# Kernel optimization log

Hardware: AMD Instinct MI355X
Metric: run time of the kernel (lower is better)

The kernel has to match this reference:

```python
import jax, jax.numpy as jnp
import numpy as np

N_NODES = 100000
N_EDGES = 500000
NODE_IN = 16
HID = 128
EDGE_IN = 1
NUM_STACKED = 4  # layers 1..4 share shapes; layer 0 maps NODE_IN -> HID


def setup_inputs() -> dict:
    key = jax.random.key(0)
    ks = jax.random.split(key, 16)

    def p(k, shape, fan_in):
        return (jax.random.normal(k, shape, dtype=jnp.float32) / np.float32(np.sqrt(fan_in)))

    inp = {}
    inp["x"] = jax.random.normal(ks[0], (N_NODES, NODE_IN), dtype=jnp.float32)
    inp["edge_index"] = jax.random.randint(ks[1], (2, N_EDGES), 0, N_NODES)
    inp["edge_attr"] = jax.random.normal(ks[2], (N_EDGES, EDGE_IN), dtype=jnp.float32)
    # GINE layer 0 (NODE_IN -> HID): edge lin maps EDGE_IN -> NODE_IN (PyG GINEConv.lin)
    inp["We0"] = p(ks[3], (EDGE_IN, NODE_IN), EDGE_IN)
    inp["be0"] = jnp.zeros((NODE_IN,), jnp.float32)
    inp["W10"] = p(ks[4], (NODE_IN, HID), NODE_IN)
    inp["b10"] = jnp.zeros((HID,), jnp.float32)
    inp["W20"] = p(ks[5], (HID, HID), HID)
    inp["b20"] = jnp.zeros((HID,), jnp.float32)
    # GINE layers 1..4 (HID -> HID), stacked on leading axis
    inp["We_s"] = p(ks[6], (NUM_STACKED, EDGE_IN, HID), EDGE_IN)
    inp["be_s"] = jnp.zeros((NUM_STACKED, HID), jnp.float32)
    inp["W1_s"] = p(ks[7], (NUM_STACKED, HID, HID), HID)
    inp["b1_s"] = jnp.zeros((NUM_STACKED, HID), jnp.float32)
    inp["W2_s"] = p(ks[8], (NUM_STACKED, HID, HID), HID)
    inp["b2_s"] = jnp.zeros((NUM_STACKED, HID), jnp.float32)
    # edge predictor: Linear(2*HID, HID) -> ELU -> Linear(HID, 1)
    inp["Wp1"] = p(ks[9], (2 * HID, HID), 2 * HID)
    inp["bp1"] = jnp.zeros((HID,), jnp.float32)
    inp["Wp2"] = p(ks[10], (HID, 1), HID)
    inp["bp2"] = jnp.zeros((1,), jnp.float32)
    return inp


def _gine(x, src, dst, eattr, We, be, W1, b1, W2, b2):
    # PyG GINEConv: aggr_i = sum_{(j->i)} ReLU(x_j + lin(edge_attr)); out = nn((1+eps)*x + aggr), eps=0
    m = jax.nn.relu(x[src] + eattr @ We + be)                 # [E, d] gathered messages
    aggr = jax.ops.segment_sum(m, dst, num_segments=x.shape[0])  # scatter-add to targets
    h = x + aggr
    return jax.nn.elu(h @ W1 + b1) @ W2 + b2                  # nn = Linear-ELU-Linear


def reference(x, edge_index, edge_attr, We0, be0, W10, b10, W20, b20,
              We_s, be_s, W1_s, b1_s, W2_s, b2_s, Wp1, bp1, Wp2, bp2):
    src, dst = edge_index[0], edge_index[1]
    # dropout is identity at inference (eval mode)
    h = jax.nn.elu(_gine(x, src, dst, edge_attr, We0, be0, W10, b10, W20, b20))
    for l in range(NUM_STACKED):
        h = jax.nn.elu(_gine(h, src, dst, edge_attr,
                             We_s[l], be_s[l], W1_s[l], b1_s[l], W2_s[l], b2_s[l]))
    ef = jnp.concatenate([h[src], h[dst]], axis=1)            # [E, 2*HID]
    out = jax.nn.elu(ef @ Wp1 + bp1) @ Wp2 + bp2              # [E, 1]
    return out[:, 0]
```

## Files before the change

kernel.cpp:

```cpp
#include <hip/hip_runtime.h>

#define N_NODES 100000
#define N_EDGES 500000
#define NODE_IN 16
#define HID 128
#define LPAD 140
#define SCAN_CHUNK 1024
#define NB_SCAN ((N_NODES + SCAN_CHUNK - 1) / SCAN_CHUNK)
#define DBINS 1024
#define NBLK64 1563
#define PERM_PAD (NBLK64 * 64)

typedef __attribute__((ext_vector_type(8))) short short8;
typedef __attribute__((ext_vector_type(4))) float f32x4;

__device__ __forceinline__ float elu_f(float v) {
    return v > 0.f ? v : __expf(v) - 1.f;
}

__device__ __forceinline__ unsigned short f2b(float f) {
    unsigned int u = __float_as_uint(f);
    unsigned int r = (u + 0x7fffu + ((u >> 16) & 1u)) >> 16;
    return (unsigned short)r;
}
__device__ __forceinline__ float b2f(unsigned short h) {
    return __uint_as_float((unsigned int)h << 16);
}
__device__ __forceinline__ unsigned short f2h(float f) {
    _Float16 h = (_Float16)f;
    unsigned short u;
    __builtin_memcpy(&u, &h, 2);
    return u;
}
__device__ __forceinline__ float h2f(unsigned short u) {
    _Float16 h;
    __builtin_memcpy(&h, &u, 2);
    return (float)h;
}

__global__ void deg_count_kernel(const int* __restrict__ ei, int* __restrict__ deg) {
    int e = blockIdx.x * 256 + threadIdx.x;
    if (e < N_EDGES) atomicAdd(&deg[ei[N_EDGES + e]], 1);
}

__global__ __launch_bounds__(1024) void scanA_kernel(const int* __restrict__ deg, int* __restrict__ bsum) {
    __shared__ int s[SCAN_CHUNK];
    int i = blockIdx.x * SCAN_CHUNK + threadIdx.x;
    s[threadIdx.x] = (i < N_NODES) ? deg[i] : 0;
    __syncthreads();
    for (int off = SCAN_CHUNK / 2; off > 0; off >>= 1) {
        if (threadIdx.x < off) s[threadIdx.x] += s[threadIdx.x + off];
        __syncthreads();
    }
    if (threadIdx.x == 0) bsum[blockIdx.x] = s[0];
}

__global__ void scanB_kernel(const int* __restrict__ bsum, int* __restrict__ boff,
                             int* __restrict__ rowPtr) {
    if (threadIdx.x == 0 && blockIdx.x == 0) {
        int r = 0;
        for (int i = 0; i < NB_SCAN; i++) { boff[i] = r; r += bsum[i]; }
        rowPtr[N_NODES] = N_EDGES;
    }
}

__global__ __launch_bounds__(1024) void scanC_kernel(const int* __restrict__ deg,
                                                     const int* __restrict__ boff,
                                                     int* __restrict__ rowPtr,
                                                     int* __restrict__ cursor) {
    __shared__ int bufA[SCAN_CHUNK], bufB[SCAN_CHUNK];
    int i = blockIdx.x * SCAN_CHUNK + threadIdx.x;
    int t = threadIdx.x;
    bufA[t] = (i < N_NODES) ? deg[i] : 0;
    __syncthreads();
    int* src = bufA; int* dst = bufB;
    for (int off = 1; off < SCAN_CHUNK; off <<= 1) {
        dst[t] = (t >= off) ? (src[t - off] + src[t]) : src[t];
        __syncthreads();
        int* tmp = src; src = dst; dst = tmp;
    }
    if (i < N_NODES) {
        int excl = (t == 0) ? 0 : src[t - 1];
        int v = excl + boff[blockIdx.x];
        rowPtr[i] = v;
        cursor[i] = v;
    }
}

__global__ void fill_kernel(const int* __restrict__ ei, const float* __restrict__ ea,
                            int* __restrict__ cursor, int2* __restrict__ edgeP) {
    int e = blockIdx.x * 256 + threadIdx.x;
    if (e < N_EDGES) {
        int d = ei[N_EDGES + e];
        int p = atomicAdd(&cursor[d], 1);
        edgeP[p] = make_int2(ei[e], __float_as_int(ea[e]));
    }
}

__global__ __launch_bounds__(1024) void s1_blockhist_kernel(const int* __restrict__ deg,
                                                            int* __restrict__ blockHist) {
    __shared__ int h[DBINS];
    int t = threadIdx.x, b = blockIdx.x;
    h[t] = 0;
    __syncthreads();
    int i = b * SCAN_CHUNK + t;
    if (i < N_NODES) atomicAdd(&h[min(deg[i], DBINS - 1)], 1);
    __syncthreads();
    blockHist[b * DBINS + t] = h[t];
}

__global__ __launch_bounds__(256) void s2a_colscan_kernel(int* __restrict__ blockHist,
                                                          int* __restrict__ binTot) {
    int k = blockIdx.x * 256 + threadIdx.x;
    if (k >= DBINS) return;
    int r = 0;
#pragma unroll 7
    for (int b = 0; b < NB_SCAN; b++) {
        int v = blockHist[b * DBINS + k];
        blockHist[b * DBINS + k] = r;
        r += v;
    }
    binTot[k] = r;
}

__global__ __launch_bounds__(1024) void s2b_binscan_kernel(const int* __restrict__ binTot,
                                                           int* __restrict__ binStart) {
    __shared__ int bufA[DBINS], bufB[DBINS];
    int k = threadIdx.x;
    bufA[k] = binTot[k];
    __syncthreads();
    int* src = bufA; int* dst = bufB;
    for (int off = 1; off < DBINS; off <<= 1) {
        dst[k] = (k >= off) ? (src[k - off] + src[k]) : src[k];
        __syncthreads();
        int* tmp = src; src = dst; dst = tmp;
    }
    binStart[k] = (k == 0) ? 0 : src[k - 1];
}

__global__ __launch_bounds__(1024) void s2c_add_kernel(int* __restrict__ blockHist,
                                                       const int* __restrict__ binStart) {
    int g = blockIdx.x * 1024 + threadIdx.x;
    if (g < NB_SCAN * DBINS) blockHist[g] += binStart[g & (DBINS - 1)];
}

__global__ __launch_bounds__(1024) void s3_scatter_kernel(const int* __restrict__ deg,
                                                          const int* __restrict__ blockHist,
                                                          int* __restrict__ perm) {
    __shared__ int cur[DBINS];
    int t = threadIdx.x, b = blockIdx.x;
    cur[t] = blockHist[b * DBINS + t];
    __syncthreads();
    int i = b * SCAN_CHUNK + t;
    if (i < N_NODES) {
        int k = min(deg[i], DBINS - 1);
        int p = atomicAdd(&cur[k], 1);
        perm[p] = i;
    }
}

__global__ __launch_bounds__(256) void pack_w_kernel(const float* __restrict__ W, int K_off,
                                                     unsigned short* __restrict__ hi,
                                                     unsigned short* __restrict__ lo)
{
    int gid = blockIdx.x * 256 + threadIdx.x;
    if (gid >= 4 * 8 * 64) return;
    int lane = gid & 63, tl = (gid >> 6) & 7, ch = gid >> 9;
    int kb = ch * 32 + (lane >> 4) * 8;
    int n  = tl * 16 + (lane & 15);
    for (int j = 0; j < 8; j++) {
        float w = W[(size_t)(K_off + kb + j) * 128 + n];
        unsigned short h = f2b(w);
        hi[(size_t)gid * 8 + j] = h;
        lo[(size_t)gid * 8 + j] = f2b(w - b2f(h));
    }
}

__global__ __launch_bounds__(256) void scatter0_kernel(
    const float* __restrict__ x, const int* __restrict__ ei,
    const float* __restrict__ ea, const float* __restrict__ We0,
    const float* __restrict__ be0, float* __restrict__ aggr)
{
    int idx = blockIdx.x * 256 + threadIdx.x;
    int e = idx >> 4, c = idx & 15;
    int s = ei[e], d = ei[N_EDGES + e];
    float m = x[s * NODE_IN + c] + ea[e] * We0[c] + be0[c];
    m = fmaxf(m, 0.f);
    atomicAdd(&aggr[d * NODE_IN + c], m);
}

__device__ __forceinline__ void fma4x4(float (&acc)[4][4],
    const float4& r0, const float4& r1, const float4& r2, const float4& r3,
    const float4& w0, const float4& w1, const float4& w2, const float4& w3)
{
    float r[4][4] = {{r0.x, r0.y, r0.z, r0.w}, {r1.x, r1.y, r1.z, r1.w},
                     {r2.x, r2.y, r2.z, r2.w}, {r3.x, r3.y, r3.z, r3.w}};
    float w[4][4] = {{w0.x, w0.y, w0.z, w0.w}, {w1.x, w1.y, w1.z, w1.w},
                     {w2.x, w2.y, w2.z, w2.w}, {w3.x, w3.y, w3.z, w3.w}};
#pragma unroll
    for (int i = 0; i < 4; i++)
#pragma unroll
        for (int k = 0; k < 4; k++)
#pragma unroll
            for (int c = 0; c < 4; c++)
                acc[i][c] = fmaf(r[i][k], w[k][c], acc[i][c]);
}

__global__ __launch_bounds__(256) void mlp0_kernel(
    const float* __restrict__ x, const float* __restrict__ aggr,
    const float* __restrict__ W1, const float* __restrict__ b1,
    const float* __restrict__ W2, const float* __restrict__ b2,
    unsigned short* __restrict__ h)
{
    __shared__ float in0[32][20];
    __shared__ float mid[32][HID];
    const int t = threadIdx.x;
    const int q = t & 31, g = t >> 5;
    const int c0 = q * 4;
    const int base = blockIdx.x * 32;

    for (int i = t; i < 32 * NODE_IN; i += 256) {
        int r = i >> 4, cc = i & 15;
        int n = base + r;
        in0[r][cc] = x[n * NODE_IN + cc] + aggr[n * NODE_IN + cc];
    }
    __syncthreads();

    float4 bb = *(const float4*)&b1[c0];
    float acc[4][4];
#pragma unroll
    for (int i = 0; i < 4; i++) { acc[i][0] = bb.x; acc[i][1] = bb.y; acc[i][2] = bb.z; acc[i][3] = bb.w; }
    for (int k = 0; k < NODE_IN; k += 4) {
        float4 r0 = *(const float4*)&in0[g * 4 + 0][k];
        float4 r1 = *(const float4*)&in0[g * 4 + 1][k];
        float4 r2 = *(const float4*)&in0[g * 4 + 2][k];
        float4 r3 = *(const float4*)&in0[g * 4 + 3][k];
        float4 w0 = *(const float4*)&W1[(k + 0) * HID + c0];
        float4 w1 = *(const float4*)&W1[(k + 1) * HID + c0];
        float4 w2 = *(const float4*)&W1[(k + 2) * HID + c0];
        float4 w3 = *(const float4*)&W1[(k + 3) * HID + c0];
        fma4x4(acc, r0, r1, r2, r3, w0, w1, w2, w3);
    }
#pragma unroll
    for (int i = 0; i < 4; i++)
        *(float4*)&mid[g * 4 + i][c0] = make_float4(elu_f(acc[i][0]), elu_f(acc[i][1]),
                                                    elu_f(acc[i][2]), elu_f(acc[i][3]));
    __syncthreads();

    float4 bb2 = *(const float4*)&b2[c0];
    float acc2[4][4];
#pragma unroll
    for (int i = 0; i < 4; i++) { acc2[i][0] = bb2.x; acc2[i][1] = bb2.y; acc2[i][2] = bb2.z; acc2[i][3] = bb2.w; }
    for (int k = 0; k < HID; k += 4) {
        float4 r0 = *(const float4*)&mid[g * 4 + 0][k];
        float4 r1 = *(const float4*)&mid[g * 4 + 1][k];
        float4 r2 = *(const float4*)&mid[g * 4 + 2][k];
        float4 r3 = *(const float4*)&mid[g * 4 + 3][k];
        float4 w0 = *(const float4*)&W2[(k + 0) * HID + c0];
        float4 w1 = *(const float4*)&W2[(k + 1) * HID + c0];
        float4 w2 = *(const float4*)&W2[(k + 2) * HID + c0];
        float4 w3 = *(const float4*)&W2[(k + 3) * HID + c0];
        fma4x4(acc2, r0, r1, r2, r3, w0, w1, w2, w3);
    }
#pragma unroll
    for (int i = 0; i < 4; i++) {
        ushort4 o;
        o.x = f2h(elu_f(acc2[i][0])); o.y = f2h(elu_f(acc2[i][1]));
        o.z = f2h(elu_f(acc2[i][2])); o.w = f2h(elu_f(acc2[i][3]));
        *(ushort4*)&h[(size_t)(base + g * 4 + i) * HID + c0] = o;
    }
}

__device__ __forceinline__ void afrag_split(const float (&buf)[16][LPAD], int lane,
                                            short8 (&ah)[4], short8 (&al)[4])
{
    const int m = lane & 15, s8 = (lane >> 4) * 8;
#pragma unroll
    for (int ch = 0; ch < 4; ch++) {
        float4 a0 = *(const float4*)&buf[m][ch * 32 + s8];
        float4 a1 = *(const float4*)&buf[m][ch * 32 + s8 + 4];
        float av[8] = {a0.x, a0.y, a0.z, a0.w, a1.x, a1.y, a1.z, a1.w};
#pragma unroll
        for (int j = 0; j < 8; j++) {
            unsigned short h = f2b(av[j]);
            ah[ch][j] = (short)h;
            al[ch][j] = (short)f2b(av[j] - b2f(h));
        }
    }
}

template <bool PRED>
__global__ __launch_bounds__(256, 4) void gine_mfma_kernel(
    const unsigned short* __restrict__ hin, const int* __restrict__ rowPtr,
    const int2* __restrict__ edgeP, const int* __restrict__ perm,
    const float* __restrict__ We, const float* __restrict__ be,
    const unsigned short* __restrict__ W1h, const unsigned short* __restrict__ W1l,
    const float* __restrict__ b1,
    const unsigned short* __restrict__ W2h, const unsigned short* __restrict__ W2l,
    const float* __restrict__ b2,
    unsigned short* __restrict__ hout,
    const unsigned short* __restrict__ P1h, const unsigned short* __restrict__ P1l,
    const unsigned short* __restrict__ P2h, const unsigned short* __restrict__ P2l,
    unsigned short* __restrict__ Pbuf)
{
    __shared__ float bufAll[4][16][LPAD];
    const int w = threadIdx.x >> 6;
    const int lane = threadIdx.x & 63;
    float (&buf)[16][LPAD] = bufAll[w];
    const int qg = lane & 15, rg = lane >> 4;
    const int c0 = qg * 8;
    const int base = blockIdx.x * 64 + w * 16;

    float wev[8], bev[8];
#pragma unroll
    for (int j = 0; j < 8; j++) { wev[j] = We[c0 + j]; bev[j] = be[c0 + j]; }

    int nn[4], s0[4], e0[4];
    float acc[4][8];
#pragma unroll
    for (int i = 0; i < 4; i++) {
        nn[i] = perm[base + rg * 4 + i];
        s0[i] = rowPtr[nn[i]];
        e0[i] = rowPtr[nn[i] + 1];
        short8 h0 = *(const short8*)&hin[(size_t)nn[i] * HID + c0];
#pragma unroll
        for (int j = 0; j < 8; j++) acc[i][j] = h2f((unsigned short)h0[j]);
    }
    int maxd = 0;
#pragma unroll
    for (int i = 0; i < 4; i++) maxd = max(maxd, e0[i] - s0[i]);

    int idx[8]; float av[8]; bool act[8];
#pragma unroll
    for (int u = 0; u < 2; u++)
#pragma unroll
        for (int i = 0; i < 4; i++) {
            int slot = u * 4 + i;
            int j = s0[i] + u;
            act[slot] = j < e0[i];
            int jc = act[slot] ? j : (N_EDGES - 1);
            int2 ep = edgeP[jc];
            idx[slot] = ep.x;
            av[slot]  = __int_as_float(ep.y);
        }

    for (int sb = 0; sb < maxd; sb += 2) {
        short8 hraw[8];
#pragma unroll
        for (int s = 0; s < 8; s++)
            hraw[s] = *(const short8*)&hin[(size_t)idx[s] * HID + c0];

        int nidx[8]; float nav[8]; bool nact[8];
#pragma unroll
        for (int u = 0; u < 2; u++)
#pragma unroll
            for (int i = 0; i < 4; i++) {
                int slot = u * 4 + i;
                int j = s0[i] + sb + 2 + u;
                nact[slot] = j < e0[i];
                int jc = nact[slot] ? j : (N_EDGES - 1);
                int2 ep = edgeP[jc];
                nidx[slot] = ep.x;
                nav[slot]  = __int_as_float(ep.y);
            }

#pragma unroll
        for (int u = 0; u < 2; u++)
#pragma unroll
            for (int i = 0; i < 4; i++) {
                int slot = u * 4 + i;
                if (act[slot]) {
#pragma unroll
                    for (int j = 0; j < 8; j++) {
                        float hv = h2f((unsigned short)hraw[slot][j]);
                        acc[i][j] += fmaxf(fmaf(av[slot], wev[j], bev[j]) + hv, 0.f);
                    }
                }
            }
#pragma unroll
        for (int s = 0; s < 8; s++) {
            idx[s] = nidx[s]; av[s] = nav[s]; act[s] = nact[s];
        }
    }
#pragma unroll
    for (int i = 0; i < 4; i++) {
        *(float4*)&buf[rg * 4 + i][c0]     = make_float4(acc[i][0], acc[i][1], acc[i][2], acc[i][3]);
        *(float4*)&buf[rg * 4 + i][c0 + 4] = make_float4(acc[i][4], acc[i][5], acc[i][6], acc[i][7]);
    }
    __syncthreads();

    const int col16 = lane & 15, r0 = (lane >> 4) * 4;

    {
        short8 ah[4], al[4];
        afrag_split(buf, lane, ah, al);
        float res[8][4];
#pragma unroll
        for (int tl = 0; tl < 8; tl++) {
            int col = tl * 16 + col16;
            float bv = b1[col];
            f32x4 c = {bv, bv, bv, bv};
#pragma unroll
            for (int ch = 0; ch < 4; ch++) {
                int off = ((ch * 8 + tl) * 64 + lane) * 8;
                short8 bh = *(const short8*)&W1h[off];
                short8 bl = *(const short8*)&W1l[off];
                c = __builtin_amdgcn_mfma_f32_16x16x32_bf16(ah[ch], bh, c, 0, 0, 0);
                c = __builtin_amdgcn_mfma_f32_16x16x32_bf16(al[ch], bh, c, 0, 0, 0);
                c = __builtin_amdgcn_mfma_f32_16x16x32_bf16(ah[ch], bl, c, 0, 0, 0);
            }
#pragma unroll
            for (int r = 0; r < 4; r++) res[tl][r] = elu_f(c[r]);
        }
        __syncthreads();
#pragma unroll
        for (int tl = 0; tl < 8; tl++)
#pragma unroll
            for (int r = 0; r < 4; r++)
                buf[r0 + r][tl * 16 + col16] = res[tl][r];
    }
    __syncthreads();

    {
        short8 ah[4], al[4];
        afrag_split(buf, lane, ah, al);
        float res[8][4];
#pragma unroll
        for (int tl = 0; tl < 8; tl++) {
            int col = tl * 16 + col16;
            float bv = b2[col];
            f32x4 c = {bv, bv, bv, bv};
#pragma unroll
            for (int ch = 0; ch < 4; ch++) {
                int off = ((ch * 8 + tl) * 64 + lane) * 8;
                short8 bh = *(const short8*)&W2h[off];
                short8 bl = *(const short8*)&W2l[off];
                c = __builtin_amdgcn_mfma_f32_16x16x32_bf16(ah[ch], bh, c, 0, 0, 0);
                c = __builtin_amdgcn_mfma_f32_16x16x32_bf16(al[ch], bh, c, 0, 0, 0);
                c = __builtin_amdgcn_mfma_f32_16x16x32_bf16(ah[ch], bl, c, 0, 0, 0);
            }
#pragma unroll
            for (int r = 0; r < 4; r++) res[tl][r] = elu_f(c[r]);
        }
        __syncthreads();
#pragma unroll
        for (int tl = 0; tl < 8; tl++)
#pragma unroll
            for (int r = 0; r < 4; r++)
                buf[r0 + r][tl * 16 + col16] = res[tl][r];
    }
    __syncthreads();

    if constexpr (!PRED) {
#pragma unroll
        for (int i = 0; i < 4; i++) {
            short8 o;
#pragma unroll
            for (int j = 0; j < 8; j++) o[j] = (short)f2h(buf[rg * 4 + i][c0 + j]);
            *(short8*)&hout[(size_t)nn[i] * HID + c0] = o;
        }
    } else {
        short8 ah[4], al[4];
        afrag_split(buf, lane, ah, al);
        int pn[4];
#pragma unroll
        for (int r = 0; r < 4; r++) pn[r] = perm[base + r0 + r];
#pragma unroll
        for (int tl = 0; tl < 8; tl++) {
            int col = tl * 16 + col16;
            f32x4 c1 = {0.f, 0.f, 0.f, 0.f};
            f32x4 c2 = {0.f, 0.f, 0.f, 0.f};
#pragma unroll
            for (int ch = 0; ch < 4; ch++) {
                int off = ((ch * 8 + tl) * 64 + lane) * 8;
                short8 bh1 = *(const short8*)&P1h[off];
                short8 bl1 = *(const short8*)&P1l[off];
                c1 = __builtin_amdgcn_mfma_f32_16x16x32_bf16(ah[ch], bh1, c1, 0, 0, 0);
                c1 = __builtin_amdgcn_mfma_f32_16x16x32_bf16(al[ch], bh1, c1, 0, 0, 0);
                c1 = __builtin_amdgcn_mfma_f32_16x16x32_bf16(ah[ch], bl1, c1, 0, 0, 0);
                short8 bh2 = *(const short8*)&P2h[off];
                short8 bl2 = *(const short8*)&P2l[off];
                c2 = __builtin_amdgcn_mfma_f32_16x16x32_bf16(ah[ch], bh2, c2, 0, 0, 0);
                c2 = __builtin_amdgcn_mfma_f32_16x16x32_bf16(al[ch], bh2, c2, 0, 0, 0);
                c2 = __builtin_amdgcn_mfma_f32_16x16x32_bf16(ah[ch], bl2, c2, 0, 0, 0);
            }
#pragma unroll
            for (int r = 0; r < 4; r++) {
                size_t n = (size_t)pn[r];
                Pbuf[n * 256 + col]       = f2b(c1[r]);
                Pbuf[n * 256 + 128 + col] = f2b(c2[r]);
            }
        }
    }
}

__global__ __launch_bounds__(256) void pred_edge_kernel(
    const unsigned short* __restrict__ Pbuf, const int* __restrict__ ei,
    const float* __restrict__ bp1, const float* __restrict__ Wp2,
    const float* __restrict__ bp2, float* __restrict__ out)
{
    const int t = threadIdx.x;
    const int lane = t & 31;
    const int eloc = t >> 5;
    const int e = blockIdx.x * 8 + eloc;
    const int c0 = lane * 4;

    int s = ei[e], d = ei[N_EDGES + e];
    ushort4 ua = *(const ushort4*)&Pbuf[(size_t)s * 256 + c0];
    ushort4 ub = *(const ushort4*)&Pbuf[(size_t)d * 256 + 128 + c0];
    float4 bb = *(const float4*)&bp1[c0];
    float4 w = *(const float4*)&Wp2[c0];
    float r = elu_f(b2f(ua.x) + b2f(ub.x) + bb.x) * w.x
            + elu_f(b2f(ua.y) + b2f(ub.y) + bb.y) * w.y
            + elu_f(b2f(ua.z) + b2f(ub.z) + bb.z) * w.z
            + elu_f(b2f(ua.w) + b2f(ub.w) + bb.w) * w.w;
#pragma unroll
    for (int off = 16; off > 0; off >>= 1) r += __shfl_down(r, off, 32);
    if (lane == 0) out[e] = r + bp2[0];
}

extern "C" void kernel_launch(void* const* d_in, const int* in_sizes, int n_in,
                              void* d_out, int out_size, void* d_ws, size_t ws_size,
                              hipStream_t stream) {
    const float* x    = (const float*)d_in[0];
    const int*   ei   = (const int*)d_in[1];
    const float* ea   = (const float*)d_in[2];
    const float* We0  = (const float*)d_in[3];
    const float* be0  = (const float*)d_in[4];
    const float* W10  = (const float*)d_in[5];
    const float* b10  = (const float*)d_in[6];
    const float* W20  = (const float*)d_in[7];
    const float* b20  = (const float*)d_in[8];
    const float* We_s = (const float*)d_in[9];
    const float* be_s = (const float*)d_in[10];
    const float* W1_s = (const float*)d_in[11];
    const float* b1_s = (const float*)d_in[12];
    const float* W2_s = (const float*)d_in[13];
    const float* b2_s = (const float*)d_in[14];
    const float* Wp1  = (const float*)d_in[15];
    const float* bp1  = (const float*)d_in[16];
    const float* Wp2  = (const float*)d_in[17];
    const float* bp2  = (const float*)d_in[18];
    float* out = (float*)d_out;

    unsigned short* h16A = (unsigned short*)d_ws;
    unsigned short* h16B = h16A + (size_t)N_NODES * HID;
    unsigned short* Pbuf = h16B + (size_t)N_NODES * HID;
    float* R = (float*)(Pbuf + (size_t)N_NODES * 256);

    float* aggr0 = R;
    int* deg     = (int*)(aggr0 + (size_t)N_NODES * NODE_IN);
    int* rowPtr  = deg + N_NODES;
    int* cursor  = rowPtr + N_NODES + 1;
    int2* edgeP  = (int2*)(cursor + N_NODES);
    int* bsum    = (int*)(edgeP + N_EDGES);
    int* boff    = bsum + NB_SCAN;
    int* perm    = boff + NB_SCAN;
    int* blockHist = perm + PERM_PAD;
    int* binTot   = blockHist + NB_SCAN * DBINS;
    int* binStart = binTot + DBINS;

    unsigned short* wpk = (unsigned short*)(R + (size_t)6 * 1024 * 1024);
    const size_t WSLOT = 16384;

    hipMemsetAsync(deg, 0, N_NODES * sizeof(int), stream);
    deg_count_kernel<<<(N_EDGES + 255) / 256, 256, 0, stream>>>(ei, deg);
    scanA_kernel<<<NB_SCAN, SCAN_CHUNK, 0, stream>>>(deg, bsum);
    scanB_kernel<<<1, 64, 0, stream>>>(bsum, boff, rowPtr);
    scanC_kernel<<<NB_SCAN, SCAN_CHUNK, 0, stream>>>(deg, boff, rowPtr, cursor);
    fill_kernel<<<(N_EDGES + 255) / 256, 256, 0, stream>>>(ei, ea, cursor, edgeP);

    hipMemsetAsync(perm, 0, PERM_PAD * sizeof(int), stream);
    s1_blockhist_kernel<<<NB_SCAN, DBINS, 0, stream>>>(deg, blockHist);
    s2a_colscan_kernel<<<4, 256, 0, stream>>>(blockHist, binTot);
    s2b_binscan_kernel<<<1, DBINS, 0, stream>>>(binTot, binStart);
    s2c_add_kernel<<<NB_SCAN, 1024, 0, stream>>>(blockHist, binStart);
    s3_scatter_kernel<<<NB_SCAN, DBINS, 0, stream>>>(deg, blockHist, perm);

    for (int l = 0; l < 4; l++) {
        pack_w_kernel<<<8, 256, 0, stream>>>(W1_s + (size_t)l * 16384, 0,
                                             wpk + (0 + l) * WSLOT, wpk + (4 + l) * WSLOT);
        pack_w_kernel<<<8, 256, 0, stream>>>(W2_s + (size_t)l * 16384, 0,
                                             wpk + (8 + l) * WSLOT, wpk + (12 + l) * WSLOT);
    }
    pack_w_kernel<<<8, 256, 0, stream>>>(Wp1, 0,   wpk + 16 * WSLOT, wpk + 17 * WSLOT);
    pack_w_kernel<<<8, 256, 0, stream>>>(Wp1, 128, wpk + 18 * WSLOT, wpk + 19 * WSLOT);

    hipMemsetAsync(aggr0, 0, (size_t)N_NODES * NODE_IN * sizeof(float), stream);
    scatter0_kernel<<<(N_EDGES * NODE_IN) / 256, 256, 0, stream>>>(x, ei, ea, We0, be0, aggr0);
    mlp0_kernel<<<N_NODES / 32, 256, 0, stream>>>(x, aggr0, W10, b10, W20, b20, h16A);

    unsigned short* hin = h16A; unsigned short* hout_ = h16B;
    for (int l = 0; l < 3; l++) {
        gine_mfma_kernel<false><<<NBLK64, 256, 0, stream>>>(
            hin, rowPtr, edgeP, perm,
            We_s + l * HID, be_s + l * HID,
            wpk + (0 + l) * WSLOT, wpk + (4 + l) * WSLOT, b1_s + l * HID,
            wpk + (8 + l) * WSLOT, wpk + (12 + l) * WSLOT, b2_s + l * HID,
            hout_, nullptr, nullptr, nullptr, nullptr, nullptr);
        unsigned short* tmp = hin; hin = hout_; hout_ = tmp;
    }

    {
        const int l = 3;
        gine_mfma_kernel<true><<<NBLK64, 256, 0, stream>>>(
            hin, rowPtr, edgeP, perm,
            We_s + l * HID, be_s + l * HID,
            wpk + (0 + l) * WSLOT, wpk + (4 + l) * WSLOT, b1_s + l * HID,
            wpk + (8 + l) * WSLOT, wpk + (12 + l) * WSLOT, b2_s + l * HID,
            nullptr, wpk + 16 * WSLOT, wpk + 17 * WSLOT,
            wpk + 18 * WSLOT, wpk + 19 * WSLOT, Pbuf);
    }

    pred_edge_kernel<<<N_EDGES / 8, 256, 0, stream>>>(Pbuf, ei, bp1, Wp2, bp2, out);
}
```

Before: 614.6 us.

## Merge weight-pack launches, fold bin offset add into scatter, deepen gather prefetch

Replaces the ten per-matrix weight-packing launches with a single kernel that covers all ten slots. Removes the separate bin-offset add kernel by adding binStart while loading the per-block cursors in the scatter kernel. In the GINE aggregation loop, each iteration now processes four edges per node instead of two, with sixteen outstanding neighbour row loads to expose more memory-level parallelism. The wider prefetch raises register pressure and may cut occupancy, and nodes with small degree do more masked work per iteration.

```diff
diff --git a/kernel.cpp b/kernel.cpp
--- a/kernel.cpp
+++ b/kernel.cpp
@@ -138,18 +138,13 @@
     binStart[k] = (k == 0) ? 0 : src[k - 1];
 }
 
-__global__ __launch_bounds__(1024) void s2c_add_kernel(int* __restrict__ blockHist,
-                                                       const int* __restrict__ binStart) {
-    int g = blockIdx.x * 1024 + threadIdx.x;
-    if (g < NB_SCAN * DBINS) blockHist[g] += binStart[g & (DBINS - 1)];
-}
-
 __global__ __launch_bounds__(1024) void s3_scatter_kernel(const int* __restrict__ deg,
                                                           const int* __restrict__ blockHist,
+                                                          const int* __restrict__ binStart,
                                                           int* __restrict__ perm) {
     __shared__ int cur[DBINS];
     int t = threadIdx.x, b = blockIdx.x;
-    cur[t] = blockHist[b * DBINS + t];
+    cur[t] = blockHist[b * DBINS + t] + binStart[t];
     __syncthreads();
     int i = b * SCAN_CHUNK + t;
     if (i < N_NODES) {
@@ -159,20 +154,28 @@
     }
 }
 
-__global__ __launch_bounds__(256) void pack_w_kernel(const float* __restrict__ W, int K_off,
-                                                     unsigned short* __restrict__ hi,
-                                                     unsigned short* __restrict__ lo)
+__global__ __launch_bounds__(256) void pack_all_kernel(
+    const float* __restrict__ W1_s, const float* __restrict__ W2_s,
+    const float* __restrict__ Wp1, unsigned short* __restrict__ wpk)
 {
     int gid = blockIdx.x * 256 + threadIdx.x;
-    if (gid >= 4 * 8 * 64) return;
-    int lane = gid & 63, tl = (gid >> 6) & 7, ch = gid >> 9;
+    if (gid >= 10 * 2048) return;
+    int m = gid >> 11, r = gid & 2047;
+    const float* W; int K_off = 0; int hi_slot, lo_slot;
+    if (m < 4)       { W = W1_s + (size_t)m * 16384;       hi_slot = m;          lo_slot = 4 + m; }
+    else if (m < 8)  { W = W2_s + (size_t)(m - 4) * 16384; hi_slot = 8 + (m - 4); lo_slot = 12 + (m - 4); }
+    else if (m == 8) { W = Wp1; K_off = 0;   hi_slot = 16; lo_slot = 17; }
+    else             { W = Wp1; K_off = 128; hi_slot = 18; lo_slot = 19; }
+    int lane = r & 63, tl = (r >> 6) & 7, ch = r >> 9;
     int kb = ch * 32 + (lane >> 4) * 8;
     int n  = tl * 16 + (lane & 15);
+    unsigned short* hi = wpk + (size_t)hi_slot * 16384;
+    unsigned short* lo = wpk + (size_t)lo_slot * 16384;
     for (int j = 0; j < 8; j++) {
         float w = W[(size_t)(K_off + kb + j) * 128 + n];
         unsigned short h = f2b(w);
-        hi[(size_t)gid * 8 + j] = h;
-        lo[(size_t)gid * 8 + j] = f2b(w - b2f(h));
+        hi[(size_t)r * 8 + j] = h;
+        lo[(size_t)r * 8 + j] = f2b(w - b2f(h));
     }
 }
 
@@ -330,9 +333,9 @@
 #pragma unroll
     for (int i = 0; i < 4; i++) maxd = max(maxd, e0[i] - s0[i]);
 
-    int idx[8]; float av[8]; bool act[8];
-#pragma unroll
-    for (int u = 0; u < 2; u++)
+    int idx[16]; float av[16]; bool act[16];
+#pragma unroll
+    for (int u = 0; u < 4; u++)
 #pragma unroll
         for (int i = 0; i < 4; i++) {
             int slot = u * 4 + i;
@@ -344,19 +347,19 @@
             av[slot]  = __int_as_float(ep.y);
         }
 
-    for (int sb = 0; sb < maxd; sb += 2) {
-        short8 hraw[8];
-#pragma unroll
-        for (int s = 0; s < 8; s++)
+    for (int sb = 0; sb < maxd; sb += 4) {
+        short8 hraw[16];
+#pragma unroll
+        for (int s = 0; s < 16; s++)
             hraw[s] = *(const short8*)&hin[(size_t)idx[s] * HID + c0];
 
-        int nidx[8]; float nav[8]; bool nact[8];
-#pragma unroll
-        for (int u = 0; u < 2; u++)
+        int nidx[16]; float nav[16]; bool nact[16];
+#pragma unroll
+        for (int u = 0; u < 4; u++)
 #pragma unroll
             for (int i = 0; i < 4; i++) {
                 int slot = u * 4 + i;
-                int j = s0[i] + sb + 2 + u;
+                int j = s0[i] + sb + 4 + u;
                 nact[slot] = j < e0[i];
                 int jc = nact[slot] ? j : (N_EDGES - 1);
                 int2 ep = edgeP[jc];
@@ -365,7 +368,7 @@
             }
 
 #pragma unroll
-        for (int u = 0; u < 2; u++)
+        for (int u = 0; u < 4; u++)
 #pragma unroll
             for (int i = 0; i < 4; i++) {
                 int slot = u * 4 + i;
@@ -378,7 +381,7 @@
                 }
             }
 #pragma unroll
-        for (int s = 0; s < 8; s++) {
+        for (int s = 0; s < 16; s++) {
             idx[s] = nidx[s]; av[s] = nav[s]; act[s] = nact[s];
         }
     }
@@ -561,7 +564,6 @@
     int* binStart = binTot + DBINS;
 
     unsigned short* wpk = (unsigned short*)(R + (size_t)6 * 1024 * 1024);
-    const size_t WSLOT = 16384;
 
     hipMemsetAsync(deg, 0, N_NODES * sizeof(int), stream);
     deg_count_kernel<<<(N_EDGES + 255) / 256, 256, 0, stream>>>(ei, deg);
@@ -574,22 +576,15 @@
     s1_blockhist_kernel<<<NB_SCAN, DBINS, 0, stream>>>(deg, blockHist);
     s2a_colscan_kernel<<<4, 256, 0, stream>>>(blockHist, binTot);
     s2b_binscan_kernel<<<1, DBINS, 0, stream>>>(binTot, binStart);
-    s2c_add_kernel<<<NB_SCAN, 1024, 0, stream>>>(blockHist, binStart);
-    s3_scatter_kernel<<<NB_SCAN, DBINS, 0, stream>>>(deg, blockHist, perm);
-
-    for (int l = 0; l < 4; l++) {
-        pack_w_kernel<<<8, 256, 0, stream>>>(W1_s + (size_t)l * 16384, 0,
-                                             wpk + (0 + l) * WSLOT, wpk + (4 + l) * WSLOT);
-        pack_w_kernel<<<8, 256, 0, stream>>>(W2_s + (size_t)l * 16384, 0,
-                                             wpk + (8 + l) * WSLOT, wpk + (12 + l) * WSLOT);
-    }
-    pack_w_kernel<<<8, 256, 0, stream>>>(Wp1, 0,   wpk + 16 * WSLOT, wpk + 17 * WSLOT);
-    pack_w_kernel<<<8, 256, 0, stream>>>(Wp1, 128, wpk + 18 * WSLOT, wpk + 19 * WSLOT);
+    s3_scatter_kernel<<<NB_SCAN, DBINS, 0, stream>>>(deg, blockHist, binStart, perm);
+
+    pack_all_kernel<<<80, 256, 0, stream>>>(W1_s, W2_s, Wp1, wpk);
 
     hipMemsetAsync(aggr0, 0, (size_t)N_NODES * NODE_IN * sizeof(float), stream);
     scatter0_kernel<<<(N_EDGES * NODE_IN) / 256, 256, 0, stream>>>(x, ei, ea, We0, be0, aggr0);
     mlp0_kernel<<<N_NODES / 32, 256, 0, stream>>>(x, aggr0, W10, b10, W20, b20, h16A);
 
+    const size_t WSLOT = 16384;
     unsigned short* hin = h16A; unsigned short* hout_ = h16B;
     for (int l = 0; l < 3; l++) {
         gine_mfma_kernel<false><<<NBLK64, 256, 0, stream>>>(
```

Result: slower. 863.6 us (+40.5%).
